# Performance work log

Hardware: AMD Instinct MI355X
Metric: run time of the kernel (lower is better)

Reference implementation:

```python
import jax, jax.numpy as jnp
import numpy as np

N_NODES = 100000
N_EDGES = 1600000
IN_CH = 64
OUT_CH = 64


def setup_inputs() -> dict:
    key = jax.random.key(0)
    k1, k2, k3, k4, k5, k6 = jax.random.split(key, 6)
    x = jax.random.normal(k1, (N_NODES, IN_CH), dtype=jnp.float32)
    edge_index = jax.random.randint(k2, (2, N_EDGES), 0, N_NODES, dtype=jnp.int64)
    edge_attr = jax.random.uniform(k3, (N_EDGES, 3), dtype=jnp.float32)
    root_weight = jax.random.normal(k4, (IN_CH, OUT_CH), dtype=jnp.float32)
    bias = jax.random.normal(k5, (OUT_CH,), dtype=jnp.float32)
    gaussian_param = jnp.ones((1,), dtype=jnp.float32)
    return {"x": x, "edge_index": edge_index, "edge_attr": edge_attr,
            "root_weight": root_weight, "bias": bias,
            "gaussian_param": gaussian_param}


def reference(x, edge_index, edge_attr, root_weight, bias, gaussian_param):
    src = edge_index[0]
    tgt = edge_index[1]
    # per-edge gaussian weight from distance (edge_attr[:, 0])
    dist = edge_attr[:, 0:1]                                  # [E, 1]
    gw = jnp.exp(-dist ** 2 / (gaussian_param ** 2 + 1e-8))   # [E, 1]
    # gather -> matmul -> scale
    messages = (x[src] @ root_weight) * gw                    # [E, out]
    # scatter-add to target nodes
    out = jax.ops.segment_sum(messages, tgt, num_segments=x.shape[0])
    out = out + x @ root_weight + bias
    return out
```

## Files before the change

kernel.cpp:

```cpp
#include <hip/hip_runtime.h>
#include <hip/hip_bf16.h>
#include <stdint.h>

#define N_NODES 100000
#define N_EDGES 1600000
#define CH 64

#define NPB 128
#define NBUCK ((N_NODES + NPB - 1) / NPB)
#define CHUNK 4096
#define BT 1024
#define EPT (CHUNK / BT)
#define NBLK_E ((N_EDGES + CHUNK - 1) / CHUNK)

#define STRIDE 2560
#define CAP 3072
#define ST 512

#define GM 64
#define NPBLK 16

typedef float f32x4 __attribute__((ext_vector_type(4)));

__device__ __forceinline__ unsigned short bf16rn(float f) {
  unsigned u = __float_as_uint(f);
  unsigned r = u + 0x7FFFu + ((u >> 16) & 1u);
  return (unsigned short)(r >> 16);
}

__device__ __forceinline__ float rdlane(float v, int l) {
  return __uint_as_float(__builtin_amdgcn_readlane(__float_as_uint(v), l));
}


__global__ __launch_bounds__(BT) void bin2_kernel(const int* __restrict__ ei,
                                                  const float* __restrict__ attr,
                                                  const float* __restrict__ gp,
                                                  int* __restrict__ gcur,
                                                  uint2* __restrict__ recs,
                                                  const float* __restrict__ x,
                                                  unsigned short* __restrict__ xh) {
  __shared__ int lhist[NBUCK];
  __shared__ int lbase[NBUCK];
  const int tid = threadIdx.x;
  for (int i = tid; i < NBUCK; i += BT) lhist[i] = 0;
  __syncthreads();
  const int cbase = blockIdx.x * CHUNK;
  const float inv = 1.0f / (gp[0] * gp[0] + 1e-8f);

  int s[EPT], t[EPT], lrank[EPT];
  float g[EPT];
#pragma unroll
  for (int k = 0; k < EPT; ++k) {
    const int e = cbase + k * BT + tid;
    if (e < N_EDGES) {
      s[k] = ei[e];
      t[k] = ei[N_EDGES + e];
      const float d = attr[3 * e];
      g[k] = __expf(-d * d * inv);
      lrank[k] = atomicAdd(&lhist[t[k] >> 7], 1);
    }
  }
  {
    const int nq = N_NODES * CH / 4;
    const int stride = gridDim.x * BT;
    for (int q = blockIdx.x * BT + tid; q < nq; q += stride) {
      const float4 v = reinterpret_cast<const float4*>(x)[q];
      ushort4 o;
      o.x = bf16rn(v.x);
      o.y = bf16rn(v.y);
      o.z = bf16rn(v.z);
      o.w = bf16rn(v.w);
      reinterpret_cast<ushort4*>(xh)[q] = o;
    }
  }
  __syncthreads();
  for (int i = tid; i < NBUCK; i += BT) {
    const int c = lhist[i];
    if (c) lbase[i] = i * STRIDE + atomicAdd(&gcur[i], c);
  }
  __syncthreads();

#pragma unroll
  for (int k = 0; k < EPT; ++k) {
    const int e = cbase + k * BT + tid;
    if (e < N_EDGES) {
      const int bb = t[k] >> 7;
      const int idx = lbase[bb] + lrank[k];
      if (idx < (bb + 1) * STRIDE) {
        uint2 rec;
        rec.x = (unsigned)s[k] | ((unsigned)(t[k] & (NPB - 1)) << 17);
        rec.y = __float_as_uint(g[k]);
        recs[idx] = rec;
      }
    }
  }
}

__global__ __launch_bounds__(ST) void sortb2_kernel(const int* __restrict__ gcur,
                                                    uint2* __restrict__ recs,
                                                    int* __restrict__ offs,
                                                    int* __restrict__ ends) {
  __shared__ uint2 srec[STRIDE];
  __shared__ int lhist[NPB];
  __shared__ int lofs[NPB];
  __shared__ int lcur[NPB];
  const int b = blockIdx.x;
  const int tid = threadIdx.x;
  const int start = b * STRIDE;
  int cnt = gcur[b];
  cnt = cnt < STRIDE ? cnt : STRIDE;

  if (tid < NPB) lhist[tid] = 0;
  __syncthreads();
  for (int i = tid; i < cnt; i += ST) {
    const uint2 r = recs[start + i];
    srec[i] = r;
    atomicAdd(&lhist[r.x >> 17], 1);
  }
  __syncthreads();
  if (tid < NPB) lofs[tid] = lhist[tid];
  __syncthreads();
  for (int off = 1; off < NPB; off <<= 1) {
    int t = 0;
    if (tid < NPB && tid >= off) t = lofs[tid - off];
    __syncthreads();
    if (tid < NPB) lofs[tid] += t;
    __syncthreads();
  }
  if (tid < NPB) {
    const int incl = lofs[tid];
    const int excl = incl - lhist[tid];
    lcur[tid] = excl;
    const int node = b * NPB + tid;
    if (node < N_NODES) {
      offs[node] = start + excl;
      ends[node] = start + incl;
    }
  }
  __syncthreads();
  for (int i = tid; i < cnt; i += ST) {
    const uint2 r = srec[i];
    const int pos = atomicAdd(&lcur[r.x >> 17], 1);
    recs[start + pos] = r;
  }
}


__global__ __launch_bounds__(BT) void hist2_kernel(const int* __restrict__ ei,
                                                   int* __restrict__ ghist,
                                                   const float* __restrict__ x,
                                                   unsigned short* __restrict__ xh,
                                                   int do_conv) {
  __shared__ int lh[NBUCK];
  const int tid = threadIdx.x;
  for (int i = tid; i < NBUCK; i += BT) lh[i] = 0;
  __syncthreads();
  const int cbase = blockIdx.x * CHUNK;
#pragma unroll
  for (int k = 0; k < EPT; ++k) {
    const int e = cbase + k * BT + tid;
    if (e < N_EDGES) atomicAdd(&lh[ei[N_EDGES + e] >> 7], 1);
  }
  if (do_conv) {
    const int nq = N_NODES * CH / 4;
    const int stride = gridDim.x * BT;
    for (int q = blockIdx.x * BT + tid; q < nq; q += stride) {
      const float4 v = reinterpret_cast<const float4*>(x)[q];
      ushort4 o;
      o.x = bf16rn(v.x);
      o.y = bf16rn(v.y);
      o.z = bf16rn(v.z);
      o.w = bf16rn(v.w);
      reinterpret_cast<ushort4*>(xh)[q] = o;
    }
  }
  __syncthreads();
  for (int i = tid; i < NBUCK; i += BT) {
    const int c = lh[i];
    if (c) atomicAdd(&ghist[i], c);
  }
}

__global__ __launch_bounds__(1024) void scan_kernel(const int* __restrict__ ghist,
                                                    int* __restrict__ gbase,
                                                    int* __restrict__ gcur) {
  __shared__ int sd[1024];
  const int tid = threadIdx.x;
  const int v = (tid < NBUCK) ? ghist[tid] : 0;
  sd[tid] = v;
  __syncthreads();
  for (int off = 1; off < 1024; off <<= 1) {
    int t = (tid >= off) ? sd[tid - off] : 0;
    __syncthreads();
    sd[tid] += t;
    __syncthreads();
  }
  if (tid < NBUCK) {
    const int excl = sd[tid] - v;
    gbase[tid] = excl;
    gcur[tid] = excl;
  }
}

__global__ __launch_bounds__(BT) void bin_kernel(const int* __restrict__ ei,
                                                 const float* __restrict__ attr,
                                                 const float* __restrict__ gp,
                                                 int* __restrict__ gcur,
                                                 uint2* __restrict__ recs) {
  __shared__ int lhist[NBUCK];
  __shared__ int lbase[NBUCK];
  const int tid = threadIdx.x;
  for (int i = tid; i < NBUCK; i += BT) lhist[i] = 0;
  __syncthreads();
  const int cbase = blockIdx.x * CHUNK;
  const float inv = 1.0f / (gp[0] * gp[0] + 1e-8f);

  int s[EPT], t[EPT], lrank[EPT];
  float g[EPT];
#pragma unroll
  for (int k = 0; k < EPT; ++k) {
    const int e = cbase + k * BT + tid;
    if (e < N_EDGES) {
      s[k] = ei[e];
      t[k] = ei[N_EDGES + e];
      const float d = attr[3 * e];
      g[k] = __expf(-d * d * inv);
      lrank[k] = atomicAdd(&lhist[t[k] >> 7], 1);
    }
  }
  __syncthreads();
  for (int i = tid; i < NBUCK; i += BT) {
    const int c = lhist[i];
    if (c) lbase[i] = atomicAdd(&gcur[i], c);
  }
  __syncthreads();

#pragma unroll
  for (int k = 0; k < EPT; ++k) {
    const int e = cbase + k * BT + tid;
    if (e < N_EDGES) {
      uint2 rec;
      rec.x = (unsigned)s[k] | ((unsigned)(t[k] & (NPB - 1)) << 17);
      rec.y = __float_as_uint(g[k]);
      recs[lbase[t[k] >> 7] + lrank[k]] = rec;
    }
  }
}

__global__ __launch_bounds__(ST) void sortb_kernel(const int* __restrict__ gbase,
                                                   const int* __restrict__ ghist,
                                                   uint2* __restrict__ recs,
                                                   int* __restrict__ offs) {
  __shared__ uint2 srec[CAP];
  __shared__ int lhist[NPB];
  __shared__ int lofs[NPB];
  __shared__ int lcur[NPB];
  const int b = blockIdx.x;
  const int tid = threadIdx.x;
  const int start = gbase[b];
  const int cnt = ghist[b] < CAP ? ghist[b] : CAP;

  if (tid < NPB) lhist[tid] = 0;
  __syncthreads();
  for (int i = tid; i < cnt; i += ST) {
    const uint2 r = recs[start + i];
    srec[i] = r;
    atomicAdd(&lhist[r.x >> 17], 1);
  }
  __syncthreads();
  if (tid < NPB) lofs[tid] = lhist[tid];
  __syncthreads();
  for (int off = 1; off < NPB; off <<= 1) {
    int t = 0;
    if (tid < NPB && tid >= off) t = lofs[tid - off];
    __syncthreads();
    if (tid < NPB) lofs[tid] += t;
    __syncthreads();
  }
  if (tid < NPB) {
    const int excl = lofs[tid] - lhist[tid];
    lcur[tid] = excl;
    const int node = b * NPB + tid;
    if (node < N_NODES) offs[node] = start + excl;
  }
  if (b == NBUCK - 1 && tid == 0) offs[N_NODES] = start + cnt;
  __syncthreads();
  for (int i = tid; i < cnt; i += ST) {
    const uint2 r = srec[i];
    const int pos = atomicAdd(&lcur[r.x >> 17], 1);
    recs[start + pos] = r;
  }
}


__global__ __launch_bounds__(1024) void reduce8h_kernel(
    const float* __restrict__ x, const unsigned short* __restrict__ xh,
    const int* __restrict__ offs, const int* __restrict__ ends,
    const uint2* __restrict__ recs, const float* __restrict__ W,
    const float* __restrict__ bias, float* __restrict__ out) {
  __shared__ float wl[CH * CH];
  __shared__ float bl[CH];
  const int tid = threadIdx.x;
  {
    const float4* W4 = reinterpret_cast<const float4*>(W);
    float4* wl4 = reinterpret_cast<float4*>(wl);
    wl4[tid] = W4[tid];
    if (tid < CH) bl[tid] = bias[tid];
  }
  __syncthreads();

  const int node = blockIdx.x * NPBLK + (tid >> 6);
  if (node >= N_NODES) return;
  const int lane = tid & 63;
  const int c2 = lane & 31;
  const int eh = lane >> 5;
  const int n0 = __builtin_amdgcn_readfirstlane(offs[node]);
  const int n1 = __builtin_amdgcn_readfirstlane(ends[node]);
  const int m = n1 - n0;

  float ax = 0.0f, ay = 0.0f;
  int j = 0;
  for (; j + 16 <= m; j += 16) {
#pragma unroll
    for (int p = 0; p < 8; ++p) {
      const uint2 r0 = recs[n0 + j + 2 * p];
      const uint2 r1 = recs[n0 + j + 2 * p + 1];
      const unsigned sx = (eh ? r1.x : r0.x) & 0x1FFFFu;
      const float g = __uint_as_float(eh ? r1.y : r0.y);
      const unsigned u =
          *reinterpret_cast<const unsigned*>(&xh[(size_t)sx * CH + c2 * 2]);
      ax += g * __uint_as_float(u << 16);
      ay += g * __uint_as_float(u & 0xFFFF0000u);
    }
  }
  for (; j + 8 <= m; j += 8) {
#pragma unroll
    for (int p = 0; p < 4; ++p) {
      const uint2 r0 = recs[n0 + j + 2 * p];
      const uint2 r1 = recs[n0 + j + 2 * p + 1];
      const unsigned sx = (eh ? r1.x : r0.x) & 0x1FFFFu;
      const float g = __uint_as_float(eh ? r1.y : r0.y);
      const unsigned u =
          *reinterpret_cast<const unsigned*>(&xh[(size_t)sx * CH + c2 * 2]);
      ax += g * __uint_as_float(u << 16);
      ay += g * __uint_as_float(u & 0xFFFF0000u);
    }
  }
  for (; j < m; j += 2) {
    const uint2 r0 = recs[n0 + j];
    uint2 r1 = {0u, 0u};
    if (j + 1 < m) r1 = recs[n0 + j + 1];
    const unsigned sx = (eh ? r1.x : r0.x) & 0x1FFFFu;
    const float g = __uint_as_float(eh ? r1.y : r0.y);
    const unsigned u =
        *reinterpret_cast<const unsigned*>(&xh[(size_t)sx * CH + c2 * 2]);
    ax += g * __uint_as_float(u << 16);
    ay += g * __uint_as_float(u & 0xFFFF0000u);
  }
  ax += __shfl_xor(ax, 32);
  ay += __shfl_xor(ay, 32);
  const float2 xv = reinterpret_cast<const float2*>(x + (size_t)node * CH)[c2];
  ax += xv.x;
  ay += xv.y;

  float a0 = 0.f, a1 = 0.f, a2 = 0.f, a3 = 0.f;
#pragma unroll
  for (int k4 = 0; k4 < CH / 4; ++k4) {
    const float s0 = rdlane(ax, 2 * k4);
    const float s1 = rdlane(ay, 2 * k4);
    const float s2 = rdlane(ax, 2 * k4 + 1);
    const float s3 = rdlane(ay, 2 * k4 + 1);
    a0 += s0 * wl[(4 * k4 + 0) * CH + lane];
    a1 += s1 * wl[(4 * k4 + 1) * CH + lane];
    a2 += s2 * wl[(4 * k4 + 2) * CH + lane];
    a3 += s3 * wl[(4 * k4 + 3) * CH + lane];
  }
  out[(size_t)node * CH + lane] = bl[lane] + ((a0 + a1) + (a2 + a3));
}

__global__ __launch_bounds__(256) void reduce3_kernel(
    const float* __restrict__ x, const int* __restrict__ offs,
    const uint2* __restrict__ recs, float* __restrict__ out) {
  const int node = (blockIdx.x * blockDim.x + threadIdx.x) >> 6;
  if (node >= N_NODES) return;
  const int lane = threadIdx.x & 63;
  const int n0 = offs[node];
  const int m = offs[node + 1] - n0;

  float acc = 0.0f;
  for (int base = 0; base < m; base += 64) {
    const int mm = (m - base) < 64 ? (m - base) : 64;
    uint2 pr = {0u, 0u};
    if (lane < mm) pr = recs[n0 + base + lane];
    const int pk_all = (int)pr.x;
    const float g_all = __uint_as_float(pr.y);
    int j = 0;
    for (; j + 4 <= mm; j += 4) {
      const int s0 = __shfl(pk_all, j + 0) & 0x1FFFF;
      const int s1 = __shfl(pk_all, j + 1) & 0x1FFFF;
      const int s2 = __shfl(pk_all, j + 2) & 0x1FFFF;
      const int s3 = __shfl(pk_all, j + 3) & 0x1FFFF;
      const float g0 = __shfl(g_all, j + 0);
      const float g1 = __shfl(g_all, j + 1);
      const float g2 = __shfl(g_all, j + 2);
      const float g3 = __shfl(g_all, j + 3);
      acc += g0 * x[(size_t)s0 * CH + lane] + g1 * x[(size_t)s1 * CH + lane] +
             g2 * x[(size_t)s2 * CH + lane] + g3 * x[(size_t)s3 * CH + lane];
    }
    for (; j < mm; ++j) {
      const int sj = __shfl(pk_all, j) & 0x1FFFF;
      const float gj = __shfl(g_all, j);
      acc += gj * x[(size_t)sj * CH + lane];
    }
  }
  out[(size_t)node * CH + lane] = acc + x[(size_t)node * CH + lane];
}

__global__ __launch_bounds__(256) void scatter_kernel(
    const float* __restrict__ x, const int* __restrict__ ei,
    const float* __restrict__ attr, const float* __restrict__ gp,
    float* __restrict__ agg) {
  const int lane = threadIdx.x & 63;
  const int wave = (blockIdx.x * blockDim.x + threadIdx.x) >> 6;
  const int nwaves = (gridDim.x * blockDim.x) >> 6;
  const float inv = 1.0f / (gp[0] * gp[0] + 1e-8f);
  for (int base = wave * 64; base < N_EDGES; base += nwaves * 64) {
    const int e = base + lane;
    const int s = ei[e];
    const int t = ei[N_EDGES + e];
    const float d = attr[3 * e];
    const float g = __expf(-d * d * inv);
#pragma unroll 1
    for (int j = 0; j < 64; ++j) {
      const int sj = __shfl(s, j);
      const int tj = __shfl(t, j);
      const float gj = __shfl(g, j);
      atomicAdd(&agg[(size_t)tj * CH + lane], gj * x[sj * CH + lane]);
    }
  }
}

__global__ __launch_bounds__(256) void rowgemm3_kernel(
    const float* __restrict__ W, const float* __restrict__ bias,
    float* __restrict__ out) {
  __shared__ float sT[64][GM + 4];
  __shared__ float wl[64 * 64];
  const int tid = threadIdx.x;
  const int node0 = blockIdx.x * GM;

  {
    const float4* W4 = reinterpret_cast<const float4*>(W);
    float4* wl4 = reinterpret_cast<float4*>(wl);
#pragma unroll
    for (int i = 0; i < 4; ++i) wl4[i * 256 + tid] = W4[i * 256 + tid];
  }
  {
    const int m = tid >> 2;
    const int kq = tid & 3;
    if (node0 + m < N_NODES) {
      const float4* r4 =
          reinterpret_cast<const float4*>(out + (size_t)(node0 + m) * CH);
#pragma unroll
      for (int q = 0; q < 4; ++q) {
        const float4 v = r4[kq * 4 + q];
        const int k = kq * 16 + q * 4;
        sT[k + 0][m] = v.x;
        sT[k + 1][m] = v.y;
        sT[k + 2][m] = v.z;
        sT[k + 3][m] = v.w;
      }
    }
  }
  __syncthreads();

  const int m0 = (tid >> 4) * 4;
  const int c0 = (tid & 15) * 4;

  const f32x4 b4 = *reinterpret_cast<const f32x4*>(&bias[c0]);
  f32x4 acc0 = b4, acc1 = b4, acc2 = b4, acc3 = b4;

#pragma unroll 8
  for (int k = 0; k < 64; ++k) {
    const f32x4 sv = *reinterpret_cast<const f32x4*>(&sT[k][m0]);
    const f32x4 wv = *reinterpret_cast<const f32x4*>(&wl[k * 64 + c0]);
    acc0 += sv.x * wv;
    acc1 += sv.y * wv;
    acc2 += sv.z * wv;
    acc3 += sv.w * wv;
  }

  __syncthreads();
  f32x4 accs[4] = {acc0, acc1, acc2, acc3};
#pragma unroll
  for (int i = 0; i < 4; ++i) {
    const int node = node0 + m0 + i;
    if (node < N_NODES)
      *reinterpret_cast<f32x4*>(&out[(size_t)node * CH + c0]) = accs[i];
  }
}

__global__ __launch_bounds__(256) void rowgemm_kernel(
    const float* __restrict__ x, const float* __restrict__ W,
    const float* __restrict__ bias, float* __restrict__ out) {
  const int r = blockIdx.x * blockDim.x + threadIdx.x;
  if (r >= N_NODES) return;
  const float* xr = x + (size_t)r * CH;
  float* outr = out + (size_t)r * CH;

  float s[CH];
#pragma unroll
  for (int k4 = 0; k4 < CH / 4; ++k4) {
    float4 xv = *reinterpret_cast<const float4*>(xr + k4 * 4);
    float4 av = *reinterpret_cast<const float4*>(outr + k4 * 4);
    s[k4 * 4 + 0] = xv.x + av.x;
    s[k4 * 4 + 1] = xv.y + av.y;
    s[k4 * 4 + 2] = xv.z + av.z;
    s[k4 * 4 + 3] = xv.w + av.w;
  }

  float acc[CH];
#pragma unroll
  for (int c = 0; c < CH; ++c) acc[c] = bias[c];

#pragma unroll
  for (int k = 0; k < CH; ++k) {
    const float sk = s[k];
#pragma unroll
    for (int c4 = 0; c4 < CH / 4; ++c4) {
      const float4 w = *reinterpret_cast<const float4*>(&W[k * CH + c4 * 4]);
      acc[c4 * 4 + 0] += sk * w.x;
      acc[c4 * 4 + 1] += sk * w.y;
      acc[c4 * 4 + 2] += sk * w.z;
      acc[c4 * 4 + 3] += sk * w.w;
    }
  }

#pragma unroll
  for (int c4 = 0; c4 < CH / 4; ++c4) {
    float4 o = {acc[c4 * 4 + 0], acc[c4 * 4 + 1], acc[c4 * 4 + 2],
                acc[c4 * 4 + 3]};
    *reinterpret_cast<float4*>(outr + c4 * 4) = o;
  }
}

extern "C" void kernel_launch(void* const* d_in, const int* in_sizes, int n_in,
                              void* d_out, int out_size, void* d_ws,
                              size_t ws_size, hipStream_t stream) {
  const float* x = (const float*)d_in[0];
  const int* ei = (const int*)d_in[1];
  const float* attr = (const float*)d_in[2];
  const float* W = (const float*)d_in[3];
  const float* bias = (const float*)d_in[4];
  const float* gp = (const float*)d_in[5];
  float* out = (float*)d_out;

  const size_t sz_i = ((size_t)NBUCK * 4 + 255) & ~(size_t)255;
  const size_t sz_xh = (size_t)N_NODES * CH * 2;
  const size_t sz_offs1 = ((size_t)N_NODES * 4 + 255) & ~(size_t)255;

  const size_t sz_recsA = (size_t)NBUCK * STRIDE * 8;
  const size_t need_fs = sz_i + sz_recsA + 2 * sz_offs1 + sz_xh;

  const size_t sz_recsB = (size_t)N_EDGES * 8;
  const size_t sz_offsB = ((size_t)(N_NODES + 1) * 4 + 255) & ~(size_t)255;
  const size_t need_b = 3 * sz_i + sz_recsB + sz_offsB;
  const size_t need_a = need_b + sz_xh;

  if (ws_size >= need_fs) {
    char* base = (char*)d_ws;
    int* gcur = (int*)base;
    uint2* recs = (uint2*)(base + sz_i);
    int* offs = (int*)(base + sz_i + sz_recsA);
    int* ends = (int*)(base + sz_i + sz_recsA + sz_offs1);
    unsigned short* xh =
        (unsigned short*)(base + sz_i + sz_recsA + 2 * sz_offs1);

    hipMemsetAsync(gcur, 0, (size_t)NBUCK * 4, stream);
    bin2_kernel<<<NBLK_E, BT, 0, stream>>>(ei, attr, gp, gcur, recs, x, xh);
    sortb2_kernel<<<NBUCK, ST, 0, stream>>>(gcur, recs, offs, ends);
    reduce8h_kernel<<<(N_NODES + NPBLK - 1) / NPBLK, 1024, 0, stream>>>(
        x, xh, offs, ends, recs, W, bias, out);
  } else if (ws_size >= need_b) {
    char* base = (char*)d_ws;
    int* ghist = (int*)base;
    int* gbase = (int*)(base + sz_i);
    int* gcur = (int*)(base + 2 * sz_i);
    uint2* recs = (uint2*)(base + 3 * sz_i);
    int* offs = (int*)(base + 3 * sz_i + sz_recsB);
    unsigned short* xh = (unsigned short*)(base + need_b);

    const int tier_a = (ws_size >= need_a) ? 1 : 0;
    hipMemsetAsync(ghist, 0, (size_t)NBUCK * 4, stream);
    hist2_kernel<<<NBLK_E, BT, 0, stream>>>(ei, ghist, x, xh, tier_a);
    scan_kernel<<<1, 1024, 0, stream>>>(ghist, gbase, gcur);
    bin_kernel<<<NBLK_E, BT, 0, stream>>>(ei, attr, gp, gcur, recs);
    sortb_kernel<<<NBUCK, ST, 0, stream>>>(gbase, ghist, recs, offs);
    if (tier_a) {
      reduce8h_kernel<<<(N_NODES + NPBLK - 1) / NPBLK, 1024, 0, stream>>>(
          x, xh, offs, offs + 1, recs, W, bias, out);
    } else {
      reduce3_kernel<<<(N_NODES * 64 + 255) / 256, 256, 0, stream>>>(x, offs,
                                                                     recs, out);
      rowgemm3_kernel<<<(N_NODES + GM - 1) / GM, 256, 0, stream>>>(W, bias,
                                                                   out);
    }
  } else {
    hipMemsetAsync(out, 0, (size_t)N_NODES * CH * sizeof(float), stream);
    scatter_kernel<<<2048, 256, 0, stream>>>(x, ei, attr, gp, out);
    rowgemm_kernel<<<(N_NODES + 255) / 256, 256, 0, stream>>>(x, W, bias, out);
  }
}
```

Baseline: 110.7 us.

## Process four nodes per wave and share W loads through LDS-transposed sums

The reduce kernel now gives each wave four nodes in sequence instead of one. It stores each node's aggregated 64-wide row (plus its own x row) transposed into a shared tile, then runs one small matmul that reuses each W element loaded from LDS across the four nodes via an f32x4 read. This replaces the per-node readlane broadcast GEMV, cutting LDS traffic and the W staging done per block, since blocks now cover 64 nodes instead of 16. In exchange each wave works through its four nodes one after another, and there are four times fewer blocks, which lowers parallelism and the latency hiding on the gather phase.

```diff
diff --git a/kernel.cpp b/kernel.cpp
--- a/kernel.cpp
+++ b/kernel.cpp
@@ -18,7 +18,7 @@
 #define ST 512
 
 #define GM 64
-#define NPBLK 16
+#define FN 64
 
 typedef float f32x4 __attribute__((ext_vector_type(4)));
 
@@ -26,10 +26,6 @@
   unsigned u = __float_as_uint(f);
   unsigned r = u + 0x7FFFu + ((u >> 16) & 1u);
   return (unsigned short)(r >> 16);
-}
-
-__device__ __forceinline__ float rdlane(float v, int l) {
-  return __uint_as_float(__builtin_amdgcn_readlane(__float_as_uint(v), l));
 }
 
 
@@ -293,12 +289,12 @@
   }
 }
 
-
-__global__ __launch_bounds__(1024) void reduce8h_kernel(
+__global__ __launch_bounds__(1024) void fusedrg_kernel(
     const float* __restrict__ x, const unsigned short* __restrict__ xh,
     const int* __restrict__ offs, const int* __restrict__ ends,
     const uint2* __restrict__ recs, const float* __restrict__ W,
     const float* __restrict__ bias, float* __restrict__ out) {
+  __shared__ float sT[CH][68];
   __shared__ float wl[CH * CH];
   __shared__ float bl[CH];
   const int tid = threadIdx.x;
@@ -310,22 +306,52 @@
   }
   __syncthreads();
 
-  const int node = blockIdx.x * NPBLK + (tid >> 6);
-  if (node >= N_NODES) return;
+  const int w = tid >> 6;
   const int lane = tid & 63;
   const int c2 = lane & 31;
   const int eh = lane >> 5;
-  const int n0 = __builtin_amdgcn_readfirstlane(offs[node]);
-  const int n1 = __builtin_amdgcn_readfirstlane(ends[node]);
-  const int m = n1 - n0;
-
-  float ax = 0.0f, ay = 0.0f;
-  int j = 0;
-  for (; j + 16 <= m; j += 16) {
-#pragma unroll
-    for (int p = 0; p < 8; ++p) {
-      const uint2 r0 = recs[n0 + j + 2 * p];
-      const uint2 r1 = recs[n0 + j + 2 * p + 1];
+  const int node0 = blockIdx.x * FN;
+
+#pragma unroll 1
+  for (int i = 0; i < 4; ++i) {
+    const int node = node0 + 4 * w + i;
+    if (node >= N_NODES) break;
+    const int n0 = __builtin_amdgcn_readfirstlane(offs[node]);
+    const int n1 = __builtin_amdgcn_readfirstlane(ends[node]);
+    const int m = n1 - n0;
+
+    float ax = 0.0f, ay = 0.0f;
+    int j = 0;
+    for (; j + 16 <= m; j += 16) {
+#pragma unroll
+      for (int p = 0; p < 8; ++p) {
+        const uint2 r0 = recs[n0 + j + 2 * p];
+        const uint2 r1 = recs[n0 + j + 2 * p + 1];
+        const unsigned sx = (eh ? r1.x : r0.x) & 0x1FFFFu;
+        const float g = __uint_as_float(eh ? r1.y : r0.y);
+        const unsigned u =
+            *reinterpret_cast<const unsigned*>(&xh[(size_t)sx * CH + c2 * 2]);
+        ax += g * __uint_as_float(u << 16);
+        ay += g * __uint_as_float(u & 0xFFFF0000u);
+      }
+    }
+    for (; j + 8 <= m; j += 8) {
+#pragma unroll
+      for (int p = 0; p < 4; ++p) {
+        const uint2 r0 = recs[n0 + j + 2 * p];
+        const uint2 r1 = recs[n0 + j + 2 * p + 1];
+        const unsigned sx = (eh ? r1.x : r0.x) & 0x1FFFFu;
+        const float g = __uint_as_float(eh ? r1.y : r0.y);
+        const unsigned u =
+            *reinterpret_cast<const unsigned*>(&xh[(size_t)sx * CH + c2 * 2]);
+        ax += g * __uint_as_float(u << 16);
+        ay += g * __uint_as_float(u & 0xFFFF0000u);
+      }
+    }
+    for (; j < m; j += 2) {
+      const uint2 r0 = recs[n0 + j];
+      uint2 r1 = {0u, 0u};
+      if (j + 1 < m) r1 = recs[n0 + j + 1];
       const unsigned sx = (eh ? r1.x : r0.x) & 0x1FFFFu;
       const float g = __uint_as_float(eh ? r1.y : r0.y);
       const unsigned u =
@@ -333,51 +359,35 @@
       ax += g * __uint_as_float(u << 16);
       ay += g * __uint_as_float(u & 0xFFFF0000u);
     }
-  }
-  for (; j + 8 <= m; j += 8) {
-#pragma unroll
-    for (int p = 0; p < 4; ++p) {
-      const uint2 r0 = recs[n0 + j + 2 * p];
-      const uint2 r1 = recs[n0 + j + 2 * p + 1];
-      const unsigned sx = (eh ? r1.x : r0.x) & 0x1FFFFu;
-      const float g = __uint_as_float(eh ? r1.y : r0.y);
-      const unsigned u =
-          *reinterpret_cast<const unsigned*>(&xh[(size_t)sx * CH + c2 * 2]);
-      ax += g * __uint_as_float(u << 16);
-      ay += g * __uint_as_float(u & 0xFFFF0000u);
-    }
-  }
-  for (; j < m; j += 2) {
-    const uint2 r0 = recs[n0 + j];
-    uint2 r1 = {0u, 0u};
-    if (j + 1 < m) r1 = recs[n0 + j + 1];
-    const unsigned sx = (eh ? r1.x : r0.x) & 0x1FFFFu;
-    const float g = __uint_as_float(eh ? r1.y : r0.y);
-    const unsigned u =
-        *reinterpret_cast<const unsigned*>(&xh[(size_t)sx * CH + c2 * 2]);
-    ax += g * __uint_as_float(u << 16);
-    ay += g * __uint_as_float(u & 0xFFFF0000u);
-  }
-  ax += __shfl_xor(ax, 32);
-  ay += __shfl_xor(ay, 32);
-  const float2 xv = reinterpret_cast<const float2*>(x + (size_t)node * CH)[c2];
-  ax += xv.x;
-  ay += xv.y;
+    ax += __shfl_xor(ax, 32);
+    ay += __shfl_xor(ay, 32);
+    if (lane < 32) {
+      const float2 xv =
+          reinterpret_cast<const float2*>(x + (size_t)node * CH)[c2];
+      sT[2 * c2][4 * w + i] = ax + xv.x;
+      sT[2 * c2 + 1][4 * w + i] = ay + xv.y;
+    }
+  }
 
   float a0 = 0.f, a1 = 0.f, a2 = 0.f, a3 = 0.f;
-#pragma unroll
-  for (int k4 = 0; k4 < CH / 4; ++k4) {
-    const float s0 = rdlane(ax, 2 * k4);
-    const float s1 = rdlane(ay, 2 * k4);
-    const float s2 = rdlane(ax, 2 * k4 + 1);
-    const float s3 = rdlane(ay, 2 * k4 + 1);
-    a0 += s0 * wl[(4 * k4 + 0) * CH + lane];
-    a1 += s1 * wl[(4 * k4 + 1) * CH + lane];
-    a2 += s2 * wl[(4 * k4 + 2) * CH + lane];
-    a3 += s3 * wl[(4 * k4 + 3) * CH + lane];
-  }
-  out[(size_t)node * CH + lane] = bl[lane] + ((a0 + a1) + (a2 + a3));
-}
+#pragma unroll 8
+  for (int k = 0; k < CH; ++k) {
+    const f32x4 sv = *reinterpret_cast<const f32x4*>(&sT[k][4 * w]);
+    const float wv = wl[k * CH + lane];
+    a0 += sv.x * wv;
+    a1 += sv.y * wv;
+    a2 += sv.z * wv;
+    a3 += sv.w * wv;
+  }
+  const float bb = bl[lane];
+  float accs[4] = {a0, a1, a2, a3};
+#pragma unroll
+  for (int i = 0; i < 4; ++i) {
+    const int node = node0 + 4 * w + i;
+    if (node < N_NODES) out[(size_t)node * CH + lane] = bb + accs[i];
+  }
+}
+
 
 __global__ __launch_bounds__(256) void reduce3_kernel(
     const float* __restrict__ x, const int* __restrict__ offs,
@@ -579,7 +589,7 @@
     hipMemsetAsync(gcur, 0, (size_t)NBUCK * 4, stream);
     bin2_kernel<<<NBLK_E, BT, 0, stream>>>(ei, attr, gp, gcur, recs, x, xh);
     sortb2_kernel<<<NBUCK, ST, 0, stream>>>(gcur, recs, offs, ends);
-    reduce8h_kernel<<<(N_NODES + NPBLK - 1) / NPBLK, 1024, 0, stream>>>(
+    fusedrg_kernel<<<(N_NODES + FN - 1) / FN, 1024, 0, stream>>>(
         x, xh, offs, ends, recs, W, bias, out);
   } else if (ws_size >= need_b) {
     char* base = (char*)d_ws;
@@ -597,7 +607,7 @@
     bin_kernel<<<NBLK_E, BT, 0, stream>>>(ei, attr, gp, gcur, recs);
     sortb_kernel<<<NBUCK, ST, 0, stream>>>(gbase, ghist, recs, offs);
     if (tier_a) {
-      reduce8h_kernel<<<(N_NODES + NPBLK - 1) / NPBLK, 1024, 0, stream>>>(
+      fusedrg_kernel<<<(N_NODES + FN - 1) / FN, 1024, 0, stream>>>(
           x, xh, offs, offs + 1, recs, W, bias, out);
     } else {
       reduce3_kernel<<<(N_NODES * 64 + 255) / 256, 256, 0, stream>>>(x, offs,
```

Result: no change. 110.2 us (-0.4%).
